# Performance work log

Hardware: AMD Instinct MI355X
Metric: run time of the kernel (lower is better)

Reference implementation:

```python
import jax, jax.numpy as jnp
import numpy as np

B, N, F, D, H, S_OBJ, S_REG, ITERS = 32, 1024, 1152, 512, 8, 8, 4, 3
S = S_OBJ + S_REG
HD = D // H
SCALE = HD ** -0.5


def ln(x, g, b, eps=1e-5):
    m = x.mean(-1, keepdims=True)
    v = ((x - m) ** 2).mean(-1, keepdims=True)
    return (x - m) / jnp.sqrt(v + eps) * g + b


def setup_inputs() -> dict:
    key = jax.random.key(0)
    ks = jax.random.split(key, 16)
    s = 0.02
    d = {
        'features': jax.random.normal(ks[0], (B, N, F), jnp.float32),
        'noise': jax.random.normal(ks[1], (B, S, D), jnp.float32),
        'w_in': jax.random.normal(ks[2], (F, D), jnp.float32) * s,
        'b_in': jnp.zeros((D,), jnp.float32),
        'ln1_g': jnp.ones((D,), jnp.float32), 'ln1_b': jnp.zeros((D,), jnp.float32),
        'slot_mu': jax.random.normal(ks[3], (1, S, D), jnp.float32) * D ** -0.5,
        'slot_log_sigma': jnp.zeros((1, S, D), jnp.float32),
        'wq': jax.random.normal(ks[4], (D, D), jnp.float32) * s,
        'wk': jax.random.normal(ks[5], (D, D), jnp.float32) * s,
        'wv': jax.random.normal(ks[6], (D, D), jnp.float32) * s,
        'gru_wih': jax.random.normal(ks[7], (D, 3 * D), jnp.float32) * s,
        'gru_whh': jax.random.normal(ks[8], (D, 3 * D), jnp.float32) * s,
        'gru_bih': jnp.zeros((3 * D,), jnp.float32),
        'gru_bhh': jnp.zeros((3 * D,), jnp.float32),
        'nslots_g': jnp.ones((D,), jnp.float32), 'nslots_b': jnp.zeros((D,), jnp.float32),
        'ninput_g': jnp.ones((D,), jnp.float32), 'ninput_b': jnp.zeros((D,), jnp.float32),
        'ffn_ln_g': jnp.ones((D,), jnp.float32), 'ffn_ln_b': jnp.zeros((D,), jnp.float32),
        'ffn_w1': jax.random.normal(ks[9], (D, 4 * D), jnp.float32) * s,
        'ffn_b1': jnp.zeros((4 * D,), jnp.float32),
        'ffn_w2': jax.random.normal(ks[10], (4 * D, D), jnp.float32) * s,
        'ffn_b2': jnp.zeros((D,), jnp.float32),
        'sel_w1': jax.random.normal(ks[11], (D, D // 2), jnp.float32) * s,
        'sel_b1': jnp.zeros((D // 2,), jnp.float32),
        'sel_w2': jax.random.normal(ks[12], (D // 2, 2), jnp.float32) * s,
        'sel_b2': jnp.zeros((2,), jnp.float32),
    }
    return d


def reference(features, noise, w_in, b_in, ln1_g, ln1_b, slot_mu, slot_log_sigma,
              wq, wk, wv, gru_wih, gru_whh, gru_bih, gru_bhh,
              nslots_g, nslots_b, ninput_g, ninput_b,
              ffn_ln_g, ffn_ln_b, ffn_w1, ffn_b1, ffn_w2, ffn_b2,
              sel_w1, sel_b1, sel_w2, sel_b2):
    b = features.shape[0]
    # input_proj: Linear + LayerNorm, then norm_input LayerNorm
    x = ln(features @ w_in + b_in, ln1_g, ln1_b)
    inp = ln(x, ninput_g, ninput_b)
    slots = slot_mu + jnp.exp(slot_log_sigma) * noise  # [B,S,D]
    k = (inp @ wk).reshape(b, N, H, HD)
    v = (inp @ wv).reshape(b, N, H, HD)
    attn_out = None
    for _ in range(ITERS):
        sn = ln(slots, nslots_g, nslots_b)
        q = (sn @ wq).reshape(b, S, H, HD)
        dots = jnp.einsum('bihd,bjhd->bihj', q, k) * SCALE  # [B,S,H,N]
        # softmax over flattened (slot, head) axis per key j
        attn = jax.nn.softmax(dots.reshape(b, S * H, N), axis=1).reshape(b, S, H, N)
        attn_out = attn.mean(axis=2)  # [B,S,N]
        attn_n = (attn + 1e-8) / (attn.sum(axis=-1, keepdims=True) + 1e-8)
        upd = jnp.einsum('bjhd,bihj->bihd', v, attn_n).reshape(b * S, D)
        h = slots.reshape(b * S, D)
        gx = upd @ gru_wih + gru_bih
        gh = h @ gru_whh + gru_bhh
        xr, xz, xn = jnp.split(gx, 3, axis=-1)
        hr, hz, hn = jnp.split(gh, 3, axis=-1)
        r = jax.nn.sigmoid(xr + hr)
        z = jax.nn.sigmoid(xz + hz)
        n = jnp.tanh(xn + r * hn)
        slots = ((1.0 - z) * n + z * h).reshape(b, S, D)
        f = ln(slots, ffn_ln_g, ffn_ln_b)
        f = jax.nn.gelu(f @ ffn_w1 + ffn_b1, approximate=False) @ ffn_w2 + ffn_b2
        slots = slots + f
    obj = slots[:, :S_OBJ]  # [B,num_slots,D]
    logits = jax.nn.relu(obj @ sel_w1 + sel_b1) @ sel_w2 + sel_b2  # [B,num_slots,2]
    decision = (jnp.argmax(logits, axis=-1) == 1).astype(slots.dtype)
    # eval-mode repair: ensure >=2 active slots per row (deterministic: first inactive)
    needed = jnp.maximum(0.0, 2.0 - decision.sum(-1, keepdims=True))
    inactive_rank = jnp.cumsum(1.0 - decision, axis=-1)
    add = ((decision == 0) & (inactive_rank <= needed)).astype(decision.dtype)
    decision = decision + add
    obj = obj * decision[..., None]
    return obj, decision, attn_out[:, :S_OBJ]
```

## Files before the change

kernel.cpp:

```cpp
#include <hip/hip_runtime.h>
#include <math.h>

typedef __attribute__((ext_vector_type(8))) short short8;
typedef __attribute__((ext_vector_type(4))) float f32x4;

typedef const __attribute__((address_space(1))) void gv_t;
typedef __attribute__((address_space(3))) void lv_t;

__device__ __forceinline__ float b2f(short u) {
  union { unsigned int i; float f; } c; c.i = ((unsigned int)(unsigned short)u) << 16; return c.f;
}
__device__ __forceinline__ short f2b(float f) {
  union { float f; unsigned int i; } c; c.f = f;
  unsigned int r = c.i + 0x7FFFu + ((c.i >> 16) & 1u);
  return (short)(r >> 16);
}
__device__ __forceinline__ void glds(const short* g, short* l) {
  __builtin_amdgcn_global_load_lds((gv_t*)g, (lv_t*)l, 16, 0, 0);
}


__global__ __launch_bounds__(256) void k_prep(
    const float* __restrict__ w_in, const float* __restrict__ wk, const float* __restrict__ wv,
    const float* __restrict__ wq, const float* __restrict__ wih, const float* __restrict__ whh,
    const float* __restrict__ bih, const float* __restrict__ bhh,
    const float* __restrict__ w1, const float* __restrict__ w2, const float* __restrict__ sl1,
    const float* __restrict__ mu, const float* __restrict__ lsig, const float* __restrict__ noise,
    const float* __restrict__ features,
    short* __restrict__ Bt1, short* __restrict__ Btkv, short* __restrict__ wq_t,
    short* __restrict__ wgru, float* __restrict__ gbias,
    short* __restrict__ w1_t, short* __restrict__ w2_t, short* __restrict__ sl1_t,
    float* __restrict__ slots, short* __restrict__ gruA, short* __restrict__ Abf)
{
  int blk = blockIdx.x, t = threadIdx.x;
  if (blk >= 2168) {
    int idx = (blk-2168)*256 + t;
    const float4* p = (const float4*)(features + (size_t)idx * 8);
    float4 a = p[0], b = p[1];
    short8 r;
    r[0]=f2b(a.x); r[1]=f2b(a.y); r[2]=f2b(a.z); r[3]=f2b(a.w);
    r[4]=f2b(b.x); r[5]=f2b(b.y); r[6]=f2b(b.z); r[7]=f2b(b.w);
    *(short8*)(Abf + (size_t)idx*8) = r;
  } else if (blk < 1392) {
    __shared__ float tile[64][68];
    int id = blk;
    const float* src = nullptr; short* dst; int Kd, n0, k0, sld = 0, sr0 = 0, sc0 = 0;
    if (id < 144) {
      dst = Bt1; Kd = 1152; n0 = (id/18)*64; k0 = (id%18)*64;
      src = w_in; sld = 512; sr0 = k0; sc0 = n0;
    } else if (id < 272) {
      id -= 144; dst = Btkv; Kd = 512; n0 = (id/8)*64; k0 = (id%8)*64;
      src = (n0 < 512) ? wk : wv; sld = 512; sr0 = k0; sc0 = n0 & 511;
    } else if (id < 336) {
      id -= 272; dst = wq_t; Kd = 512; n0 = (id/8)*64; k0 = (id%8)*64;
      src = wq; sld = 512; sr0 = k0; sc0 = n0;
    } else if (id < 848) {
      id -= 336; dst = wgru; Kd = 1024; n0 = (id/16)*64; k0 = (id%16)*64;
      int g = n0 >> 9, c0 = n0 & 511; bool hi = (k0 >= 512);
      sld = 1536; sr0 = hi ? k0 - 512 : k0;
      if (g == 0)      { src = hi ? whh : wih; sc0 = c0; }
      else if (g == 1) { src = hi ? whh : wih; sc0 = 512 + c0; }
      else if (g == 2) { src = hi ? nullptr : wih; sc0 = 1024 + c0; }
      else             { src = hi ? whh : nullptr; sc0 = 1024 + c0; }
    } else if (id < 1104) {
      id -= 848; dst = w1_t; Kd = 512; n0 = (id/8)*64; k0 = (id%8)*64;
      src = w1; sld = 2048; sr0 = k0; sc0 = n0;
    } else if (id < 1360) {
      id -= 1104; dst = w2_t; Kd = 2048; n0 = (id/32)*64; k0 = (id%32)*64;
      src = w2; sld = 512; sr0 = k0; sc0 = n0;
    } else {
      id -= 1360; dst = sl1_t; Kd = 512; n0 = (id/8)*64; k0 = (id%8)*64;
      src = sl1; sld = 256; sr0 = k0; sc0 = n0;
    }
    if (src) {
      #pragma unroll
      for (int i = 0; i < 4; ++i) {
        int kk = (t >> 4) + i*16, nn = (t & 15) * 4;
        *(float4*)&tile[kk][nn] = *(const float4*)(src + (size_t)(sr0+kk)*sld + sc0 + nn);
      }
    } else {
      #pragma unroll
      for (int i = 0; i < 4; ++i) {
        int kk = (t >> 4) + i*16, nn = (t & 15) * 4;
        tile[kk][nn] = 0.f; tile[kk][nn+1] = 0.f; tile[kk][nn+2] = 0.f; tile[kk][nn+3] = 0.f;
      }
    }
    __syncthreads();
    #pragma unroll
    for (int i = 0; i < 2; ++i) {
      int c = i*256 + t;
      int row = c >> 3, off = (c & 7) * 8;
      short8 o;
      #pragma unroll
      for (int e = 0; e < 8; ++e) o[e] = f2b(tile[off+e][row]);
      *(short8*)(dst + (size_t)(n0+row)*Kd + k0 + off) = o;
    }
  } else if (blk < 1400) {
    int n = (blk-1392)*256 + t;
    int g = n >> 9;
    float v;
    if (g <= 1)      v = bih[n] + bhh[n];
    else if (g == 2) v = bih[n];
    else             v = bhh[1024 + (n - 1536)];
    gbias[n] = v;
  } else {
    int idx = (blk-1400)*256 + t;
    int sd = idx % 6144;
    float v = mu[sd] + __expf(lsig[sd]) * noise[idx];
    slots[idx] = v;
    int row = idx >> 9, c = idx & 511;
    gruA[(size_t)row*1024 + 512 + c] = f2b(v);
  }
}


__global__ __launch_bounds__(256) void gemm_p(
    const short* __restrict__ A, const short* __restrict__ Bt,
    const float* __restrict__ bias, short* __restrict__ Cb,
    int N, int K, int lda, int ldb)
{
  __shared__ short As[2][128*64];
  __shared__ short Bs[2][128*64];
  const int t = threadIdx.x;
  const int lane = t & 63, wave = t >> 6;

  const int nwg = gridDim.x, gridX = N >> 7, orig = blockIdx.x;
  const int q = nwg >> 3, r = nwg & 7, xcd = orig & 7, base = orig >> 3;
  const int wgid = (xcd < r ? xcd*(q+1) : r*(q+1) + (xcd - r)*q) + base;
  const int bx = wgid % gridX, by = wgid / gridX;

  const int rowBase = by * 128, colBase = bx * 128;
  const int wm = (wave >> 1) * 64, wn = (wave & 1) * 64;
  const int fr = lane & 15, kcf = lane >> 4;
  f32x4 acc[4][4] = {};

  int srow[4], scol[4];
  #pragma unroll
  for (int i = 0; i < 4; ++i) {
    int c = i*256 + t;
    srow[i] = c >> 3;
    scol[i] = ((c & 7) ^ (srow[i] & 7)) * 8;
  }

  const int nsteps = K >> 6;
  auto STAGE = [&](int step, int buf) {
    int kb = step * 64;
    #pragma unroll
    for (int i = 0; i < 4; ++i) {
      int c = i*256 + t;
      glds(A + (size_t)(rowBase + srow[i])*lda + kb + scol[i], As[buf] + c*8);
      glds(Bt + (size_t)(colBase + srow[i])*ldb + kb + scol[i], Bs[buf] + c*8);
    }
  };

  STAGE(0, 0);
  if (nsteps > 1) { STAGE(1, 1); asm volatile("s_waitcnt vmcnt(8)" ::: "memory"); }
  else            {              asm volatile("s_waitcnt vmcnt(0)" ::: "memory"); }
  __builtin_amdgcn_sched_barrier(0);
  __builtin_amdgcn_s_barrier();
  __builtin_amdgcn_sched_barrier(0);

  for (int tt = 0; tt < nsteps; ++tt) {
    const int cur = tt & 1;
    short8 af[2][4], bf[2][4];
    #pragma unroll
    for (int ks = 0; ks < 2; ++ks) {
      int kc = ks*4 + kcf;
      #pragma unroll
      for (int m = 0; m < 4; ++m) {
        int rowa = wm + m*16 + fr;
        af[ks][m] = *(const short8*)(As[cur] + rowa*64 + (kc ^ (rowa & 7))*8);
        int rowb = wn + m*16 + fr;
        bf[ks][m] = *(const short8*)(Bs[cur] + rowb*64 + (kc ^ (rowb & 7))*8);
      }
    }
    asm volatile("s_waitcnt lgkmcnt(0)" ::: "memory");
    __builtin_amdgcn_sched_barrier(0);
    __builtin_amdgcn_s_barrier();
    __builtin_amdgcn_sched_barrier(0);
    if (tt + 2 < nsteps) STAGE(tt + 2, cur);
    #pragma unroll
    for (int ks = 0; ks < 2; ++ks)
      #pragma unroll
      for (int m = 0; m < 4; ++m)
        #pragma unroll
        for (int n = 0; n < 4; ++n)
          acc[m][n] = __builtin_amdgcn_mfma_f32_16x16x32_bf16(af[ks][m], bf[ks][n], acc[m][n], 0, 0, 0);
    if (tt + 1 < nsteps) {
      if (tt + 2 < nsteps) asm volatile("s_waitcnt vmcnt(8)" ::: "memory");
      else                 asm volatile("s_waitcnt vmcnt(0)" ::: "memory");
      __builtin_amdgcn_sched_barrier(0);
      __builtin_amdgcn_s_barrier();
      __builtin_amdgcn_sched_barrier(0);
    }
  }

  const int cr = (lane >> 4) * 4, cc2 = lane & 15;
  #pragma unroll
  for (int m = 0; m < 4; ++m)
    #pragma unroll
    for (int n = 0; n < 4; ++n) {
      int col = colBase + wn + n*16 + cc2;
      float bv = bias ? bias[col] : 0.f;
      #pragma unroll
      for (int j = 0; j < 4; ++j) {
        int row = rowBase + wm + m*16 + cr + j;
        Cb[(size_t)row*N + col] = f2b(acc[m][n][j] + bv);
      }
    }
}


template<int ACT, bool OUTBF, bool SPLITK>
__global__ __launch_bounds__(256) void gemm_t(
    const short* __restrict__ A, const short* __restrict__ Bt,
    const float* __restrict__ bias,
    float* __restrict__ Cf, short* __restrict__ Cb,
    int N, int Kp, int lda, int ldb, int ldf, int ldcb, int cboff, int skstride)
{
  __shared__ short As[128*64];
  __shared__ short Bs[128*64];
  const int t = threadIdx.x;
  const int lane = t & 63, wave = t >> 6;

  const int nwg = gridDim.x, gridX = N >> 7, orig = blockIdx.x;
  const int q = nwg >> 3, r = nwg & 7, xcd = orig & 7, base = orig >> 3;
  const int wgid = (xcd < r ? xcd*(q+1) : r*(q+1) + (xcd - r)*q) + base;
  const int bx = wgid % gridX, by = wgid / gridX;

  const int rowBase = by * 128, colBase = bx * 128;
  const size_t koff = (size_t)blockIdx.y * Kp;
  const int wm = (wave >> 1) * 64, wn = (wave & 1) * 64;
  const int fr = lane & 15, kcf = lane >> 4;
  f32x4 acc[4][4] = {};

  int srow[4], scol[4];
  #pragma unroll
  for (int i = 0; i < 4; ++i) {
    int c = i*256 + t;
    srow[i] = c >> 3;
    scol[i] = ((c & 7) ^ (srow[i] & 7)) * 8;
  }

  for (int kb = 0; kb < Kp; kb += 64) {
    __syncthreads();
    #pragma unroll
    for (int i = 0; i < 4; ++i) {
      int c = i*256 + t;
      glds(A + (size_t)(rowBase + srow[i])*lda + koff + kb + scol[i], As + c*8);
      glds(Bt + (size_t)(colBase + srow[i])*ldb + koff + kb + scol[i], Bs + c*8);
    }
    __syncthreads();
    #pragma unroll
    for (int ks = 0; ks < 2; ++ks) {
      short8 af[4], bf[4];
      #pragma unroll
      for (int m = 0; m < 4; ++m) {
        int row = wm + m*16 + fr;
        int kc = ks*4 + kcf;
        af[m] = *(const short8*)(As + row*64 + (kc ^ (row & 7))*8);
      }
      #pragma unroll
      for (int n = 0; n < 4; ++n) {
        int row = wn + n*16 + fr;
        int kc = ks*4 + kcf;
        bf[n] = *(const short8*)(Bs + row*64 + (kc ^ (row & 7))*8);
      }
      #pragma unroll
      for (int m = 0; m < 4; ++m)
        #pragma unroll
        for (int n = 0; n < 4; ++n)
          acc[m][n] = __builtin_amdgcn_mfma_f32_16x16x32_bf16(af[m], bf[n], acc[m][n], 0, 0, 0);
    }
  }

  const int cr = (lane >> 4) * 4, cc2 = lane & 15;
  if (SPLITK) {
    float* dst = Cf + (size_t)blockIdx.y * skstride;
    #pragma unroll
    for (int m = 0; m < 4; ++m)
      #pragma unroll
      for (int n = 0; n < 4; ++n) {
        int col = colBase + wn + n*16 + cc2;
        #pragma unroll
        for (int j = 0; j < 4; ++j) {
          int row = rowBase + wm + m*16 + cr + j;
          dst[(size_t)row * ldf + col] = acc[m][n][j];
        }
      }
  } else {
    #pragma unroll
    for (int m = 0; m < 4; ++m)
      #pragma unroll
      for (int n = 0; n < 4; ++n) {
        int col = colBase + wn + n*16 + cc2;
        float bv = bias ? bias[col] : 0.f;
        #pragma unroll
        for (int j = 0; j < 4; ++j) {
          int row = rowBase + wm + m*16 + cr + j;
          float v = acc[m][n][j] + bv;
          if (ACT == 1) v = 0.5f*v*(1.f + erff(v*0.70710678118f));
          else if (ACT == 2) v = fmaxf(v, 0.f);
          if (OUTBF) Cb[(size_t)row*ldcb + cboff + col] = f2b(v);
          else Cf[(size_t)row*ldf + col] = v;
        }
      }
  }
}


__global__ __launch_bounds__(256) void k_gruln(const float* __restrict__ p, const float* __restrict__ gbias,
    float* __restrict__ slots, short* __restrict__ fln,
    const float* __restrict__ g, const float* __restrict__ bb)
{
  int t = threadIdx.x, lane = t & 63;
  int row = blockIdx.x*4 + (t >> 6);
  int c = lane * 8;
  float g0[8], g1[8], g2[8], g3[8];
  *(float4*)g0     = *(const float4*)(gbias + c);
  *(float4*)(g0+4) = *(const float4*)(gbias + c + 4);
  *(float4*)g1     = *(const float4*)(gbias + 512 + c);
  *(float4*)(g1+4) = *(const float4*)(gbias + 512 + c + 4);
  *(float4*)g2     = *(const float4*)(gbias + 1024 + c);
  *(float4*)(g2+4) = *(const float4*)(gbias + 1024 + c + 4);
  *(float4*)g3     = *(const float4*)(gbias + 1536 + c);
  *(float4*)(g3+4) = *(const float4*)(gbias + 1536 + c + 4);
  const float* base = p + (size_t)row*2048 + c;
  #pragma unroll
  for (int s = 0; s < 4; ++s) {
    const float* qq = base + (size_t)s*786432;
    #pragma unroll
    for (int gi = 0; gi < 4; ++gi) {
      float* dst = (gi == 0) ? g0 : (gi == 1) ? g1 : (gi == 2) ? g2 : g3;
      float4 a = *(const float4*)(qq + gi*512), b4 = *(const float4*)(qq + gi*512 + 4);
      dst[0]+=a.x; dst[1]+=a.y; dst[2]+=a.z; dst[3]+=a.w;
      dst[4]+=b4.x; dst[5]+=b4.y; dst[6]+=b4.z; dst[7]+=b4.w;
    }
  }
  float hold[8], v[8];
  *(float4*)hold     = *(const float4*)(slots + (size_t)row*512 + c);
  *(float4*)(hold+4) = *(const float4*)(slots + (size_t)row*512 + c + 4);
  #pragma unroll
  for (int e = 0; e < 8; ++e) {
    float r = 1.f/(1.f+__expf(-g0[e]));
    float z = 1.f/(1.f+__expf(-g1[e]));
    float n = tanhf(g2[e] + r*g3[e]);
    v[e] = (1.f-z)*n + z*hold[e];
  }
  *(float4*)(slots + (size_t)row*512 + c)     = *(float4*)v;
  *(float4*)(slots + (size_t)row*512 + c + 4) = *(float4*)(v+4);
  float s1 = 0.f, s2 = 0.f;
  #pragma unroll
  for (int e = 0; e < 8; ++e) { s1 += v[e]; s2 += v[e]*v[e]; }
  #pragma unroll
  for (int m = 1; m < 64; m <<= 1) { s1 += __shfl_xor(s1, m, 64); s2 += __shfl_xor(s2, m, 64); }
  float mean = s1 * (1.f/512.f);
  float rs = rsqrtf(s2*(1.f/512.f) - mean*mean + 1e-5f);
  short8 o;
  #pragma unroll
  for (int e = 0; e < 8; ++e) o[e] = f2b((v[e]-mean)*rs*g[c+e] + bb[c+e]);
  *(short8*)(fln + (size_t)row*512 + c) = o;
}


__global__ __launch_bounds__(256) void k_ffn2redln(const float* __restrict__ p, const float* __restrict__ b2,
    float* __restrict__ slots, short* __restrict__ gruA, short* __restrict__ sn,
    const float* __restrict__ g, const float* __restrict__ bb)
{
  int t = threadIdx.x, lane = t & 63;
  int row = blockIdx.x*4 + (t >> 6);
  int c = lane * 8;
  size_t base = (size_t)row*512 + c;
  float v[8];
  *(float4*)v     = *(const float4*)(slots + base);
  *(float4*)(v+4) = *(const float4*)(slots + base + 4);
  #pragma unroll
  for (int e = 0; e < 8; ++e) v[e] += b2[c+e];
  #pragma unroll
  for (int s = 0; s < 8; ++s) {
    const float* qq = p + (size_t)s*196608 + base;
    float4 a = *(const float4*)qq, b4 = *(const float4*)(qq+4);
    v[0]+=a.x; v[1]+=a.y; v[2]+=a.z; v[3]+=a.w;
    v[4]+=b4.x; v[5]+=b4.y; v[6]+=b4.z; v[7]+=b4.w;
  }
  *(float4*)(slots + base)     = *(float4*)v;
  *(float4*)(slots + base + 4) = *(float4*)(v+4);
  short8 o;
  #pragma unroll
  for (int e = 0; e < 8; ++e) o[e] = f2b(v[e]);
  *(short8*)(gruA + (size_t)row*1024 + 512 + c) = o;
  float s1 = 0.f, s2 = 0.f;
  #pragma unroll
  for (int e = 0; e < 8; ++e) { s1 += v[e]; s2 += v[e]*v[e]; }
  #pragma unroll
  for (int m = 1; m < 64; m <<= 1) { s1 += __shfl_xor(s1, m, 64); s2 += __shfl_xor(s2, m, 64); }
  float mean = s1 * (1.f/512.f);
  float rs = rsqrtf(s2*(1.f/512.f) - mean*mean + 1e-5f);
  short8 o2;
  #pragma unroll
  for (int e = 0; e < 8; ++e) o2[e] = f2b((v[e]-mean)*rs*g[c+e] + bb[c+e]);
  *(short8*)(sn + base) = o2;
}


__global__ __launch_bounds__(256) void k_ffn1red(const float* __restrict__ p, const float* __restrict__ b1,
                                                 short* __restrict__ f1) {
  int i = blockIdx.x*256 + threadIdx.x;
  int col = (i*8) & 2047;
  float v[8], w[8];
  *(float4*)v = *(const float4*)(p + (size_t)i*8);
  *(float4*)(v+4) = *(const float4*)(p + (size_t)i*8 + 4);
  const float* p2 = p + 786432;
  *(float4*)w = *(const float4*)(p2 + (size_t)i*8);
  *(float4*)(w+4) = *(const float4*)(p2 + (size_t)i*8 + 4);
  short8 o;
  #pragma unroll
  for (int e = 0; e < 8; ++e) {
    float x = v[e] + w[e] + b1[col + e];
    x = 0.5f*x*(1.f + erff(x*0.70710678118f));
    o[e] = f2b(x);
  }
  *(short8*)(f1 + (size_t)i*8) = o;
}


__global__ __launch_bounds__(256) void k_ln2(const short* __restrict__ y, short* __restrict__ inp,
    const float* __restrict__ g1, const float* __restrict__ b1,
    const float* __restrict__ g2, const float* __restrict__ b2)
{
  int t = threadIdx.x, lane = t & 63;
  int row = blockIdx.x * 4 + (t >> 6);
  const short8 raw = *(const short8*)(y + (size_t)row*512 + lane*8);
  float x[8];
  #pragma unroll
  for (int e = 0; e < 8; ++e) x[e] = b2f(raw[e]);
  float s = 0.f, ss = 0.f;
  #pragma unroll
  for (int e = 0; e < 8; ++e) { s += x[e]; ss += x[e]*x[e]; }
  #pragma unroll
  for (int m = 1; m < 64; m <<= 1) { s += __shfl_xor(s, m, 64); ss += __shfl_xor(ss, m, 64); }
  float mean = s * (1.f/512.f);
  float rs = rsqrtf(ss*(1.f/512.f) - mean*mean + 1e-5f);
  int c = lane * 8;
  #pragma unroll
  for (int e = 0; e < 8; ++e) x[e] = (x[e]-mean)*rs*g1[c+e] + b1[c+e];
  s = 0.f; ss = 0.f;
  #pragma unroll
  for (int e = 0; e < 8; ++e) { s += x[e]; ss += x[e]*x[e]; }
  #pragma unroll
  for (int m = 1; m < 64; m <<= 1) { s += __shfl_xor(s, m, 64); ss += __shfl_xor(ss, m, 64); }
  float mean2 = s * (1.f/512.f);
  float rs2 = rsqrtf(ss*(1.f/512.f) - mean2*mean2 + 1e-5f);
  short8 o;
  #pragma unroll
  for (int e = 0; e < 8; ++e) o[e] = f2b((x[e]-mean2)*rs2*g2[c+e] + b2[c+e]);
  *(short8*)(inp + (size_t)row*512 + lane*8) = o;
}


__global__ __launch_bounds__(256) void k_lnb(const float* __restrict__ x, short* __restrict__ out,
    const float* __restrict__ g, const float* __restrict__ b)
{
  int t = threadIdx.x, lane = t & 63;
  int row = blockIdx.x * 4 + (t >> 6);
  const float* src = x + (size_t)row*512 + lane*8;
  float v[8];
  *(float4*)v = *(const float4*)src;
  *(float4*)(v+4) = *(const float4*)(src+4);
  float s = 0.f, ss = 0.f;
  #pragma unroll
  for (int e = 0; e < 8; ++e) { s += v[e]; ss += v[e]*v[e]; }
  #pragma unroll
  for (int m = 1; m < 64; m <<= 1) { s += __shfl_xor(s, m, 64); ss += __shfl_xor(ss, m, 64); }
  float mean = s * (1.f/512.f);
  float rs = rsqrtf(ss*(1.f/512.f) - mean*mean + 1e-5f);
  int c = lane * 8;
  short8 o;
  #pragma unroll
  for (int e = 0; e < 8; ++e) o[e] = f2b((v[e]-mean)*rs*g[c+e] + b[c+e]);
  *(short8*)(out + (size_t)row*512 + c) = o;
}


__global__ __launch_bounds__(256) void k_attn(
    const float* __restrict__ qparts, const short* __restrict__ kv,
    float* __restrict__ pvp, float* __restrict__ denp, float* __restrict__ aout)
{
  __shared__ float qs[12][512];
  __shared__ float ksh[128][65];
  __shared__ float dots[96][132];
  const int t = threadIdx.x;
  const int jt = blockIdx.x, b = blockIdx.y;

  for (int i = t; i < 6144; i += 256) {
    int s = i >> 9, d = i & 511;
    size_t o = (size_t)(b*12+s)*512 + d;
    qs[s][d] = qparts[o] + qparts[196608 + o] + qparts[393216 + o] + qparts[589824 + o];
  }

  const int jj = t & 127, sg = t >> 7;
  for (int h = 0; h < 8; ++h) {
    __syncthreads();
    #pragma unroll
    for (int i = 0; i < 4; ++i) {
      int c = i*256 + t;
      int j2 = c >> 3, seg = (c & 7) * 8;
      short8 raw = *(const short8*)(kv + ((size_t)(b*1024 + jt*128 + j2))*1024 + h*64 + seg);
      #pragma unroll
      for (int e = 0; e < 8; ++e) ksh[j2][seg+e] = b2f(raw[e]);
    }
    __syncthreads();
    float d6[6] = {};
    for (int d = 0; d < 64; ++d) {
      float kvv = ksh[jj][d];
      #pragma unroll
      for (int i = 0; i < 6; ++i) d6[i] += qs[sg*6+i][h*64+d] * kvv;
    }
    #pragma unroll
    for (int i = 0; i < 6; ++i) dots[(sg*6+i)*8 + h][jj] = d6[i] * 0.125f;
  }
  __syncthreads();

  {
    int j = t >> 1, half = (t & 1) * 48;
    float mx = -1e30f;
    #pragma unroll
    for (int i = 0; i < 48; ++i) mx = fmaxf(mx, dots[half+i][j]);
    mx = fmaxf(mx, __shfl_xor(mx, 1, 64));
    float ex[48];
    float sum = 0.f;
    #pragma unroll
    for (int i = 0; i < 48; ++i) { ex[i] = __expf(dots[half+i][j] - mx); sum += ex[i]; }
    sum += __shfl_xor(sum, 1, 64);
    float inv = 1.f / sum;
    float as_[6] = {0,0,0,0,0,0};
    #pragma unroll
    for (int i = 0; i < 48; ++i) {
      float a = ex[i] * inv;
      dots[half+i][j] = a;
      as_[i >> 3] += a;
    }
    if (aout) {
      int sbase = (t & 1) * 6;
      #pragma unroll
      for (int q2 = 0; q2 < 6; ++q2) {
        int s = sbase + q2;
        if (s < 8) aout[((size_t)(b*8+s))*1024 + jt*128 + j] = as_[q2] * 0.125f;
      }
    }
  }

  const int d = t & 63, sq = t >> 6;
  for (int h = 0; h < 8; ++h) {
    __syncthreads();
    #pragma unroll
    for (int i = 0; i < 4; ++i) {
      int c = i*256 + t;
      int j2 = c >> 3, seg = (c & 7) * 8;
      short8 raw = *(const short8*)(kv + ((size_t)(b*1024 + jt*128 + j2))*1024 + 512 + h*64 + seg);
      #pragma unroll
      for (int e = 0; e < 8; ++e) ksh[j2][seg+e] = b2f(raw[e]);
    }
    __syncthreads();
    float a3[3] = {0.f, 0.f, 0.f};
    for (int j2 = 0; j2 < 128; ++j2) {
      float vv = ksh[j2][d];
      #pragma unroll
      for (int i = 0; i < 3; ++i) a3[i] += dots[(sq + 4*i)*8 + h][j2] * vv;
    }
    #pragma unroll
    for (int i = 0; i < 3; ++i)
      pvp[((size_t)(jt*32+b))*6144 + (sq + 4*i)*512 + h*64 + d] = a3[i];
    if (t < 12) {
      float ls = 0.f;
      for (int j2 = 0; j2 < 128; ++j2) ls += dots[t*8 + h][j2];
      denp[((size_t)(jt*32+b))*96 + t*8 + h] = ls;
    }
  }
}


__global__ __launch_bounds__(256) void k_pvred(const float* __restrict__ pvp, const float* __restrict__ denp,
                                               short* __restrict__ gruA)
{
  __shared__ float den[96];
  int t = threadIdx.x, b = blockIdx.x;
  if (t < 96) {
    float s = 0.f;
    #pragma unroll
    for (int jt2 = 0; jt2 < 8; ++jt2) s += denp[((size_t)(jt2*32+b))*96 + t];
    den[t] = s + 1e-8f;
  }
  __syncthreads();
  for (int i = t; i < 6144; i += 256) {
    int s = i >> 9, rem = i & 511, h = rem >> 6;
    float acc = 0.f;
    #pragma unroll
    for (int jt2 = 0; jt2 < 8; ++jt2) acc += pvp[((size_t)(jt2*32+b))*6144 + i];
    gruA[((size_t)(b*12+s))*1024 + rem] = f2b(acc / den[s*8 + h]);
  }
}


__global__ __launch_bounds__(64) void k_decide(const float* __restrict__ hid, const float* __restrict__ w2,
    const float* __restrict__ b2, const float* __restrict__ slots, float* __restrict__ out)
{
  __shared__ float lg[16];
  __shared__ float dec[8];
  int b = blockIdx.x, t = threadIdx.x;
  if (t < 16) {
    int s = t >> 1, cl = t & 1;
    const float* hr = hid + (size_t)(b*12+s)*256;
    float a = b2[cl];
    for (int k = 0; k < 256; ++k) a += hr[k] * w2[k*2+cl];
    lg[t] = a;
  }
  __syncthreads();
  if (t == 0) {
    float d0[8]; float tot = 0.f;
    #pragma unroll
    for (int s = 0; s < 8; ++s) { d0[s] = (lg[2*s+1] > lg[2*s]) ? 1.f : 0.f; tot += d0[s]; }
    float needed = fmaxf(0.f, 2.f - tot);
    float cum = 0.f;
    #pragma unroll
    for (int s = 0; s < 8; ++s) {
      cum += 1.f - d0[s];
      float add = (d0[s] == 0.f && cum <= needed) ? 1.f : 0.f;
      float dd = d0[s] + add;
      dec[s] = dd;
      out[131072 + b*8 + s] = dd;
    }
  }
  __syncthreads();
  for (int i = 0; i < 64; ++i) {
    int idx = i*64 + t;
    int s = idx >> 9, c = idx & 511;
    out[(size_t)(b*8+s)*512 + c] = slots[(size_t)(b*12+s)*512 + c] * dec[s];
  }
}


extern "C" void kernel_launch(void* const* d_in, const int* in_sizes, int n_in,
                              void* d_out, int out_size, void* d_ws, size_t ws_size,
                              hipStream_t stream) {
  const float* features = (const float*)d_in[0];
  const float* noise    = (const float*)d_in[1];
  const float* w_in     = (const float*)d_in[2];
  const float* b_in     = (const float*)d_in[3];
  const float* ln1_g    = (const float*)d_in[4];
  const float* ln1_b    = (const float*)d_in[5];
  const float* slot_mu  = (const float*)d_in[6];
  const float* slot_ls  = (const float*)d_in[7];
  const float* wq       = (const float*)d_in[8];
  const float* wk       = (const float*)d_in[9];
  const float* wv       = (const float*)d_in[10];
  const float* gru_wih  = (const float*)d_in[11];
  const float* gru_whh  = (const float*)d_in[12];
  const float* gru_bih  = (const float*)d_in[13];
  const float* gru_bhh  = (const float*)d_in[14];
  const float* nslots_g = (const float*)d_in[15];
  const float* nslots_b = (const float*)d_in[16];
  const float* ninput_g = (const float*)d_in[17];
  const float* ninput_b = (const float*)d_in[18];
  const float* ffnln_g  = (const float*)d_in[19];
  const float* ffnln_b  = (const float*)d_in[20];
  const float* ffn_w1   = (const float*)d_in[21];
  const float* ffn_b1   = (const float*)d_in[22];
  const float* ffn_w2   = (const float*)d_in[23];
  const float* ffn_b2   = (const float*)d_in[24];
  const float* sel_w1   = (const float*)d_in[25];
  const float* sel_b1   = (const float*)d_in[26];
  const float* sel_w2   = (const float*)d_in[27];
  const float* sel_b2   = (const float*)d_in[28];
  float* out = (float*)d_out;
  float* fnull = (float*)nullptr;
  short* snull = (short*)nullptr;

  char* w = (char*)d_ws;
  size_t off = 0;
  auto alloc = [&](size_t n) { char* p = w + off; off = (off + n + 255) & ~255ULL; return p; };
  short* Abf   = (short*)alloc(75497472);
  short* kv    = Abf;
  short* ybf   = (short*)alloc(33554432);
  short* inp   = (short*)alloc(33554432);
  short* Bt1   = (short*)alloc(1179648);
  short* Btkv  = (short*)alloc(1048576);
  short* wq_t  = (short*)alloc(524288);
  short* wgru  = (short*)alloc(4194304);
  float* gbias = (float*)alloc(8192);
  short* w1_t  = (short*)alloc(2097152);
  short* w2_t  = (short*)alloc(2097152);
  short* sl1_t = (short*)alloc(262144);
  float* slots = (float*)alloc(786432);
  short* gruA  = (short*)alloc(786432);
  short* sn    = (short*)alloc(393216);
  float* parts = (float*)alloc(12582912);
  float* pvp   = (float*)alloc(6291456);
  float* denp  = (float*)alloc(98304);
  short* fln   = (short*)alloc(393216);
  short* f1    = (short*)alloc(1572864);
  float* hid   = (float*)alloc(393216);
  (void)ws_size; (void)in_sizes; (void)n_in; (void)out_size;

  k_prep<<<dim3(20600), dim3(256), 0, stream>>>(
      w_in, wk, wv, wq, gru_wih, gru_whh, gru_bih, gru_bhh,
      ffn_w1, ffn_w2, sel_w1, slot_mu, slot_ls, noise, features,
      Bt1, Btkv, wq_t, wgru, gbias, w1_t, w2_t, sl1_t, slots, gruA, Abf);

  gemm_p<<<dim3(1024), dim3(256), 0, stream>>>(Abf, Bt1, b_in, ybf, 512, 1152, 1152, 1152);
  k_ln2<<<dim3(8192), dim3(256), 0, stream>>>(ybf, inp, ln1_g, ln1_b, ninput_g, ninput_b);
  gemm_p<<<dim3(2048), dim3(256), 0, stream>>>(inp, Btkv, fnull, kv, 1024, 512, 512, 512);

  k_lnb<<<dim3(96), dim3(256), 0, stream>>>(slots, sn, nslots_g, nslots_b);

  for (int it = 0; it < 3; ++it) {
    gemm_t<0,false,true><<<dim3(12, 4), dim3(256), 0, stream>>>(
        sn, wq_t, fnull, parts, snull, 512, 128, 512, 512, 512, 0, 0, 196608);
    k_attn<<<dim3(8, 32), dim3(256), 0, stream>>>(parts, kv, pvp, denp,
        it == 2 ? out + 131328 : fnull);
    k_pvred<<<dim3(32), dim3(256), 0, stream>>>(pvp, denp, gruA);
    gemm_t<0,false,true><<<dim3(48, 4), dim3(256), 0, stream>>>(
        gruA, wgru, fnull, parts, snull, 2048, 256, 1024, 1024, 2048, 0, 0, 786432);
    k_gruln<<<dim3(96), dim3(256), 0, stream>>>(parts, gbias, slots, fln, ffnln_g, ffnln_b);
    gemm_t<0,false,true><<<dim3(48, 2), dim3(256), 0, stream>>>(
        fln, w1_t, fnull, parts, snull, 2048, 256, 512, 512, 2048, 0, 0, 786432);
    k_ffn1red<<<dim3(384), dim3(256), 0, stream>>>(parts, ffn_b1, f1);
    gemm_t<0,false,true><<<dim3(12, 8), dim3(256), 0, stream>>>(
        f1, w2_t, fnull, parts, snull, 512, 256, 2048, 2048, 512, 0, 0, 196608);
    k_ffn2redln<<<dim3(96), dim3(256), 0, stream>>>(parts, ffn_b2, slots, gruA, sn,
        nslots_g, nslots_b);
  }

  gemm_t<2,false,false><<<dim3(6), dim3(256), 0, stream>>>(
      gruA + 512, sl1_t, sel_b1, hid, snull, 256, 512, 1024, 512, 256, 0, 0, 0);
  k_decide<<<dim3(32), dim3(64), 0, stream>>>(hid, sel_w2, sel_b2, slots, out);
}
```

Before: 520.3 us.

## Double-buffer gemm_t LDS loads and spread small row kernels across more blocks

gemm_t now double-buffers its A/B LDS tiles, prefetching two k-steps ahead with explicit vmcnt waits and barriers, so global loads overlap the MFMA work. The row-wise LN/GRU/FFN reduction kernels switch from four rows per 256-thread block to one row per 64-thread block, launching four times as many workgroups. The attention kernel gets an XCD-aware block remap, and k_pvred is split across 8 chunks per batch for more parallelism. The costs are doubled LDS use per GEMM block, which may lower occupancy, and more hand-scheduled synchronisation that is fragile.

```diff
diff --git a/kernel.cpp b/kernel.cpp
--- a/kernel.cpp
+++ b/kernel.cpp
@@ -218,8 +218,8 @@
     float* __restrict__ Cf, short* __restrict__ Cb,
     int N, int Kp, int lda, int ldb, int ldf, int ldcb, int cboff, int skstride)
 {
-  __shared__ short As[128*64];
-  __shared__ short Bs[128*64];
+  __shared__ short As[2][128*64];
+  __shared__ short Bs[2][128*64];
   const int t = threadIdx.x;
   const int lane = t & 63, wave = t >> 6;
 
@@ -242,35 +242,56 @@
     scol[i] = ((c & 7) ^ (srow[i] & 7)) * 8;
   }
 
-  for (int kb = 0; kb < Kp; kb += 64) {
-    __syncthreads();
+  const int nsteps = Kp >> 6;
+  auto STAGE = [&](int step, int buf) {
+    int kb = step * 64;
     #pragma unroll
     for (int i = 0; i < 4; ++i) {
       int c = i*256 + t;
-      glds(A + (size_t)(rowBase + srow[i])*lda + koff + kb + scol[i], As + c*8);
-      glds(Bt + (size_t)(colBase + srow[i])*ldb + koff + kb + scol[i], Bs + c*8);
-    }
-    __syncthreads();
+      glds(A + (size_t)(rowBase + srow[i])*lda + koff + kb + scol[i], As[buf] + c*8);
+      glds(Bt + (size_t)(colBase + srow[i])*ldb + koff + kb + scol[i], Bs[buf] + c*8);
+    }
+  };
+
+  STAGE(0, 0);
+  if (nsteps > 1) { STAGE(1, 1); asm volatile("s_waitcnt vmcnt(8)" ::: "memory"); }
+  else            {              asm volatile("s_waitcnt vmcnt(0)" ::: "memory"); }
+  __builtin_amdgcn_sched_barrier(0);
+  __builtin_amdgcn_s_barrier();
+  __builtin_amdgcn_sched_barrier(0);
+
+  for (int tt = 0; tt < nsteps; ++tt) {
+    const int cur = tt & 1;
+    short8 af[2][4], bf[2][4];
     #pragma unroll
     for (int ks = 0; ks < 2; ++ks) {
-      short8 af[4], bf[4];
+      int kc = ks*4 + kcf;
       #pragma unroll
       for (int m = 0; m < 4; ++m) {
-        int row = wm + m*16 + fr;
-        int kc = ks*4 + kcf;
-        af[m] = *(const short8*)(As + row*64 + (kc ^ (row & 7))*8);
+        int rowa = wm + m*16 + fr;
+        af[ks][m] = *(const short8*)(As[cur] + rowa*64 + (kc ^ (rowa & 7))*8);
+        int rowb = wn + m*16 + fr;
+        bf[ks][m] = *(const short8*)(Bs[cur] + rowb*64 + (kc ^ (rowb & 7))*8);
       }
-      #pragma unroll
-      for (int n = 0; n < 4; ++n) {
-        int row = wn + n*16 + fr;
-        int kc = ks*4 + kcf;
-        bf[n] = *(const short8*)(Bs + row*64 + (kc ^ (row & 7))*8);
-      }
+    }
+    asm volatile("s_waitcnt lgkmcnt(0)" ::: "memory");
+    __builtin_amdgcn_sched_barrier(0);
+    __builtin_amdgcn_s_barrier();
+    __builtin_amdgcn_sched_barrier(0);
+    if (tt + 2 < nsteps) STAGE(tt + 2, cur);
+    #pragma unroll
+    for (int ks = 0; ks < 2; ++ks)
       #pragma unroll
       for (int m = 0; m < 4; ++m)
         #pragma unroll
         for (int n = 0; n < 4; ++n)
-          acc[m][n] = __builtin_amdgcn_mfma_f32_16x16x32_bf16(af[m], bf[n], acc[m][n], 0, 0, 0);
+          acc[m][n] = __builtin_amdgcn_mfma_f32_16x16x32_bf16(af[ks][m], bf[ks][n], acc[m][n], 0, 0, 0);
+    if (tt + 1 < nsteps) {
+      if (tt + 2 < nsteps) asm volatile("s_waitcnt vmcnt(8)" ::: "memory");
+      else                 asm volatile("s_waitcnt vmcnt(0)" ::: "memory");
+      __builtin_amdgcn_sched_barrier(0);
+      __builtin_amdgcn_s_barrier();
+      __builtin_amdgcn_sched_barrier(0);
     }
   }
 
@@ -309,12 +330,12 @@
 }
 
 
-__global__ __launch_bounds__(256) void k_gruln(const float* __restrict__ p, const float* __restrict__ gbias,
+__global__ __launch_bounds__(64) void k_gruln(const float* __restrict__ p, const float* __restrict__ gbias,
     float* __restrict__ slots, short* __restrict__ fln,
     const float* __restrict__ g, const float* __restrict__ bb)
 {
-  int t = threadIdx.x, lane = t & 63;
-  int row = blockIdx.x*4 + (t >> 6);
+  int lane = threadIdx.x;
+  int row = blockIdx.x;
   int c = lane * 8;
   float g0[8], g1[8], g2[8], g3[8];
   *(float4*)g0     = *(const float4*)(gbias + c);
@@ -363,12 +384,12 @@
 }
 
 
-__global__ __launch_bounds__(256) void k_ffn2redln(const float* __restrict__ p, const float* __restrict__ b2,
+__global__ __launch_bounds__(64) void k_ffn2redln(const float* __restrict__ p, const float* __restrict__ b2,
     float* __restrict__ slots, short* __restrict__ gruA, short* __restrict__ sn,
     const float* __restrict__ g, const float* __restrict__ bb)
 {
-  int t = threadIdx.x, lane = t & 63;
-  int row = blockIdx.x*4 + (t >> 6);
+  int lane = threadIdx.x;
+  int row = blockIdx.x;
   int c = lane * 8;
   size_t base = (size_t)row*512 + c;
   float v[8];
@@ -458,11 +479,11 @@
 }
 
 
-__global__ __launch_bounds__(256) void k_lnb(const float* __restrict__ x, short* __restrict__ out,
+__global__ __launch_bounds__(64) void k_lnb(const float* __restrict__ x, short* __restrict__ out,
     const float* __restrict__ g, const float* __restrict__ b)
 {
-  int t = threadIdx.x, lane = t & 63;
-  int row = blockIdx.x * 4 + (t >> 6);
+  int lane = threadIdx.x;
+  int row = blockIdx.x;
   const float* src = x + (size_t)row*512 + lane*8;
   float v[8];
   *(float4*)v = *(const float4*)src;
@@ -490,7 +511,9 @@
   __shared__ float ksh[128][65];
   __shared__ float dots[96][132];
   const int t = threadIdx.x;
-  const int jt = blockIdx.x, b = blockIdx.y;
+  const int orig = blockIdx.x;
+  const int wgid = (orig & 7) * 32 + (orig >> 3);
+  const int b = wgid >> 3, jt = wgid & 7;
 
   for (int i = t; i < 6144; i += 256) {
     int s = i >> 9, d = i & 511;
@@ -584,7 +607,7 @@
                                                short* __restrict__ gruA)
 {
   __shared__ float den[96];
-  int t = threadIdx.x, b = blockIdx.x;
+  int t = threadIdx.x, chunk = blockIdx.x, b = blockIdx.y;
   if (t < 96) {
     float s = 0.f;
     #pragma unroll
@@ -592,7 +615,9 @@
     den[t] = s + 1e-8f;
   }
   __syncthreads();
-  for (int i = t; i < 6144; i += 256) {
+  int i = chunk*768 + t;
+  #pragma unroll
+  for (int k = 0; k < 3; ++k, i += 256) {
     int s = i >> 9, rem = i & 511, h = rem >> 6;
     float acc = 0.f;
     #pragma unroll
@@ -711,23 +736,23 @@
   k_ln2<<<dim3(8192), dim3(256), 0, stream>>>(ybf, inp, ln1_g, ln1_b, ninput_g, ninput_b);
   gemm_p<<<dim3(2048), dim3(256), 0, stream>>>(inp, Btkv, fnull, kv, 1024, 512, 512, 512);
 
-  k_lnb<<<dim3(96), dim3(256), 0, stream>>>(slots, sn, nslots_g, nslots_b);
+  k_lnb<<<dim3(384), dim3(64), 0, stream>>>(slots, sn, nslots_g, nslots_b);
 
   for (int it = 0; it < 3; ++it) {
     gemm_t<0,false,true><<<dim3(12, 4), dim3(256), 0, stream>>>(
         sn, wq_t, fnull, parts, snull, 512, 128, 512, 512, 512, 0, 0, 196608);
-    k_attn<<<dim3(8, 32), dim3(256), 0, stream>>>(parts, kv, pvp, denp,
+    k_attn<<<dim3(256), dim3(256), 0, stream>>>(parts, kv, pvp, denp,
         it == 2 ? out + 131328 : fnull);
-    k_pvred<<<dim3(32), dim3(256), 0, stream>>>(pvp, denp, gruA);
+    k_pvred<<<dim3(8, 32), dim3(256), 0, stream>>>(pvp, denp, gruA);
     gemm_t<0,false,true><<<dim3(48, 4), dim3(256), 0, stream>>>(
         gruA, wgru, fnull, parts, snull, 2048, 256, 1024, 1024, 2048, 0, 0, 786432);
-    k_gruln<<<dim3(96), dim3(256), 0, stream>>>(parts, gbias, slots, fln, ffnln_g, ffnln_b);
+    k_gruln<<<dim3(384), dim3(64), 0, stream>>>(parts, gbias, slots, fln, ffnln_g, ffnln_b);
     gemm_t<0,false,true><<<dim3(48, 2), dim3(256), 0, stream>>>(
         fln, w1_t, fnull, parts, snull, 2048, 256, 512, 512, 2048, 0, 0, 786432);
     k_ffn1red<<<dim3(384), dim3(256), 0, stream>>>(parts, ffn_b1, f1);
     gemm_t<0,false,true><<<dim3(12, 8), dim3(256), 0, stream>>>(
         f1, w2_t, fnull, parts, snull, 512, 256, 2048, 2048, 512, 0, 0, 196608);
-    k_ffn2redln<<<dim3(96), dim3(256), 0, stream>>>(parts, ffn_b2, slots, gruA, sn,
+    k_ffn2redln<<<dim3(384), dim3(64), 0, stream>>>(parts, ffn_b2, slots, gruA, sn,
         nslots_g, nslots_b);
   }
 
```

Measured after the change: 479.5 us (median of 2 runs). 1.09x faster.
